# Kernel optimization log

Measured on AMD Instinct MI355X. Metric: run time of the kernel, lower is better.

## Reference

```python
import jax, jax.numpy as jnp
import numpy as np

N_ENT = 50000     # n_entities
C = 128           # channel
N_EDGES = 1600000 # n_edges (avg degree 32)
N_REL = 11        # n_relations; edge_type in [1, N_REL-1]
N_HOPS = 3
EPS = 1e-12       # F.normalize default eps


def setup_inputs() -> dict:
    key = jax.random.key(0)
    k1, k2, k3, k4 = jax.random.split(key, 4)
    entity_emb = jax.random.normal(k1, (N_ENT, C), dtype=jnp.float32)
    edge_index = jax.random.randint(k2, (2, N_EDGES), 0, N_ENT, dtype=jnp.int64)
    edge_type = jax.random.randint(k3, (N_EDGES,), 1, N_REL, dtype=jnp.int64)
    # xavier_uniform bound for (N_REL-1, C)
    bound = float(np.sqrt(6.0 / ((N_REL - 1) + C)))
    weight = jax.random.uniform(k4, (N_REL - 1, C), jnp.float32, -bound, bound)
    return {"entity_emb": entity_emb, "edge_index": edge_index,
            "edge_type": edge_type, "weight": weight}


def reference(entity_emb, edge_index, edge_type, weight):
    head, tail = edge_index[0], edge_index[1]
    # relation embedding per edge: weight[edge_type - 1] -> [E, C]
    rel_emb = weight[edge_type - 1]
    ones = jnp.ones((edge_index.shape[1],), entity_emb.dtype)
    # per-head in-degree counts (constant across hops)
    cnt = jax.ops.segment_sum(ones, head, num_segments=N_ENT)
    denom = jnp.maximum(cnt, 1.0)[:, None]  # scatter_mean: zero rows stay zero

    def hop(emb):
        msg = emb[tail] * rel_emb                                   # gather + mul [E, C]
        agg = jax.ops.segment_sum(msg, head, num_segments=N_ENT) / denom  # scatter_mean
        # F.normalize (L2 per row)
        norm = jnp.linalg.norm(agg, axis=1, keepdims=True)
        return agg / jnp.maximum(norm, EPS)

    res = entity_emb
    emb = entity_emb
    for _ in range(N_HOPS):
        emb = hop(emb)
        res = res + emb
    return res
```

## Files before the change

### kernel.cpp

```cpp
#include <hip/hip_runtime.h>

#define N_ENT   50000
#define CH      128
#define N_EDGES 1600000
#define N_RELM1 10
#define NB      391
#define BCAP    4608
#define PART_BLOCKS 800
#define CHUNK   (N_EDGES / PART_BLOCKS)
#define EPS_N   1e-12f

__device__ __forceinline__ unsigned int f2bf_bits(float f) {
    unsigned int x = __float_as_uint(f);
    return (x + 0x7FFFu + ((x >> 16) & 1u)) >> 16;
}

__global__ __launch_bounds__(256) void gc_part_kernel(const int* __restrict__ head,
                                                      const int* __restrict__ tail,
                                                      const int* __restrict__ etyp,
                                                      int* __restrict__ barr,
                                                      int* __restrict__ pack,
                                                      const float* __restrict__ ent,
                                                      unsigned int* __restrict__ emb) {
    __shared__ int hist[512];
    __shared__ int boff_s[512];
    __shared__ int fctr[512];
    __shared__ int psum[256];
    __shared__ int stageE[CHUNK];
    __shared__ unsigned short stageB[CHUNK];
    __shared__ int stage2[CHUNK];
    int tid = threadIdx.x, blk = blockIdx.x;
    for (int i = tid; i < 512; i += 256) { hist[i] = 0; fctr[i] = 0; }
    __syncthreads();
    int lo = blk * CHUNK;
    for (int i = tid; i < CHUNK; i += 256) {
        int e = lo + i;
        int h = head[e];
        int b = h >> 7;
        stageE[i] = (tail[e] & 0xFFFF) | ((etyp[e] - 1) << 16) | ((h & 127) << 20);
        stageB[i] = (unsigned short)b;
        atomicAdd(&hist[b], 1);
    }
    __syncthreads();
    int a0 = hist[2 * tid], a1 = hist[2 * tid + 1];
    int s2 = a0 + a1;
    psum[tid] = s2;
    __syncthreads();
    for (int d = 1; d < 256; d <<= 1) {
        int t = (tid >= d) ? psum[tid - d] : 0;
        __syncthreads();
        psum[tid] += t;
        __syncthreads();
    }
    int excl = psum[tid] - s2;
    boff_s[2 * tid] = excl;
    boff_s[2 * tid + 1] = excl + a0;
    __syncthreads();
    for (int i = tid; i < CHUNK; i += 256) {
        int b = stageB[i];
        int pos = boff_s[b] + atomicAdd(&fctr[b], 1);
        stage2[pos] = stageE[i];
    }
    __syncthreads();
    for (int i = tid; i < CHUNK; i += 256) barr[lo + i] = stage2[i];
    for (int i = tid; i < NB; i += 256)
        pack[blk * NB + i] = (boff_s[i] << 8) | fctr[i];
    for (int i = blk * 256 + tid; i < N_ENT * (CH / 2); i += PART_BLOCKS * 256) {
        float2 v = *(const float2*)(ent + 2 * (size_t)i);
        emb[i] = f2bf_bits(v.x) | (f2bf_bits(v.y) << 16);
    }
}

__global__ __launch_bounds__(1024) void gc_place_kernel(const int* __restrict__ barr,
                                                        const int* __restrict__ pack,
                                                        unsigned int* __restrict__ off_deg,
                                                        int* __restrict__ csr) {
    __shared__ int ent_s[BCAP];
    __shared__ int psum[1024];
    __shared__ int hcnt[128];
    __shared__ int hloc[128];
    __shared__ int hctr[128];
    int b = blockIdx.x, tid = threadIdx.x;
    if (tid < 128) { hcnt[tid] = 0; hctr[tid] = 0; }
    int c = 0, o = 0;
    if (tid < PART_BLOCKS) {
        int pk = pack[tid * NB + b];
        c = pk & 255;
        o = pk >> 8;
    }
    psum[tid] = c;
    __syncthreads();
    for (int d = 1; d < 1024; d <<= 1) {
        int t = (tid >= d) ? psum[tid - d] : 0;
        __syncthreads();
        psum[tid] += t;
        __syncthreads();
    }
    int my_off = psum[tid] - c;
    int n = psum[1023];
    const int* src = barr + tid * CHUNK + o;
    for (int k = 0; k < c; ++k) ent_s[my_off + k] = src[k];
    __syncthreads();
    for (int i = tid; i < n; i += 1024)
        atomicAdd(&hcnt[(ent_s[i] >> 20) & 127], 1);
    __syncthreads();
    int v = (tid < 128) ? hcnt[tid] : 0;
    for (int d = 1; d < 128; d <<= 1) {
        int t = (tid < 128 && tid >= d) ? hcnt[tid - d] : 0;
        __syncthreads();
        if (tid < 128) hcnt[tid] += t;
        __syncthreads();
    }
    int lo = b * BCAP;
    if (tid < 128) {
        int start = lo + hcnt[tid] - v;
        hloc[tid] = start;
        int h = (b << 7) + tid;
        if (h < N_ENT) off_deg[h] = ((unsigned)start << 11) | (unsigned)v;
    }
    __syncthreads();
    for (int i = tid; i < n; i += 1024) {
        int e = ent_s[i];
        int hl = (e >> 20) & 127;
        int pos = hloc[hl] + atomicAdd(&hctr[hl], 1);
        csr[pos] = e & 0xFFFFF;
    }
}

__global__ __launch_bounds__(256) void gc_hop_kernel(
        const unsigned int* __restrict__ src,
        const unsigned int* __restrict__ off_deg,
        const int* __restrict__ csr,
        const float* __restrict__ wt,
        unsigned int* __restrict__ dst,
        float* __restrict__ res,
        const float* __restrict__ ent,
        int init) {
    __shared__ float wt_s[N_RELM1 * CH];
    for (int i = threadIdx.x; i < N_RELM1 * CH; i += 256) wt_s[i] = wt[i];
    __syncthreads();

    int wave = threadIdx.x >> 6, lane = threadIdx.x & 63;
    int row = __builtin_amdgcn_readfirstlane(blockIdx.x * 4 + wave);

    unsigned od = (unsigned)__builtin_amdgcn_readfirstlane((int)off_deg[row]);
    int seg = (int)(od >> 11);
    int deg = (int)(od & 2047u);
    int seg_end = seg + deg;

    float ax = 0.f, ay = 0.f;
    int j = seg;
    for (; j + 8 <= seg_end; j += 8) {
        int pk[8];
        #pragma unroll
        for (int u = 0; u < 8; ++u)
            pk[u] = __builtin_amdgcn_readfirstlane(csr[j + u]);
        #pragma unroll
        for (int u = 0; u < 8; ++u) {
            unsigned v = src[pk[u] % 65536 * 64 + lane];
            float2 w = *(const float2*)(&wt_s[(pk[u] >> 16) * CH + 2 * lane]);
            ax = fmaf(__uint_as_float(v << 16), w.x, ax);
            ay = fmaf(__uint_as_float(v & 0xFFFF0000u), w.y, ay);
        }
    }
    for (; j < seg_end; ++j) {
        int pk = __builtin_amdgcn_readfirstlane(csr[j]);
        unsigned v = src[pk % 65536 * 64 + lane];
        float2 w = *(const float2*)(&wt_s[(pk >> 16) * CH + 2 * lane]);
        ax = fmaf(__uint_as_float(v << 16), w.x, ax);
        ay = fmaf(__uint_as_float(v & 0xFFFF0000u), w.y, ay);
    }

    float invd = 1.0f / fmaxf((float)deg, 1.0f);
    float x0 = ax * invd, x1 = ay * invd;

    float s = x0 * x0 + x1 * x1;
    #pragma unroll
    for (int o = 32; o > 0; o >>= 1) s += __shfl_down(s, o, 64);
    s = __shfl(s, 0, 64);

    float inv = 1.0f / fmaxf(sqrtf(s), EPS_N);
    float y0 = x0 * inv, y1 = x1 * inv;

    dst[(row << 6) + lane] = f2bf_bits(y0) | (f2bf_bits(y1) << 16);

    int base = (row << 7) + 2 * lane;
    if (init) {
        float2 e = *(const float2*)(ent + base);
        *(float2*)(res + base) = make_float2(e.x + y0, e.y + y1);
    } else {
        float2 rv = *(const float2*)(res + base);
        *(float2*)(res + base) = make_float2(rv.x + y0, rv.y + y1);
    }
}

extern "C" void kernel_launch(void* const* d_in, const int* in_sizes, int n_in,
                              void* d_out, int out_size, void* d_ws, size_t ws_size,
                              hipStream_t stream) {
    const float* ent  = (const float*)d_in[0];
    const int*   eidx = (const int*)d_in[1];
    const int*   etyp = (const int*)d_in[2];
    const float* wt   = (const float*)d_in[3];
    float*       res  = (float*)d_out;

    const int* head = eidx;
    const int* tail = eidx + N_EDGES;

    unsigned int* embA = (unsigned int*)d_ws;
    unsigned int* embB = embA + (size_t)N_ENT * 64;
    int* barr  = (int*)(embB + (size_t)N_ENT * 64);
    int* pack  = barr + N_EDGES;
    unsigned int* off_deg = (unsigned int*)(pack + PART_BLOCKS * NB);
    int* csr   = (int*)(off_deg + N_ENT);

    gc_part_kernel<<<PART_BLOCKS, 256, 0, stream>>>(head, tail, etyp, barr, pack,
                                                    ent, embA);
    gc_place_kernel<<<NB, 1024, 0, stream>>>(barr, pack, off_deg, csr);

    const int hop_grid = N_ENT / 4;
    gc_hop_kernel<<<hop_grid, 256, 0, stream>>>(embA, off_deg, csr, wt, embB, res, ent, 1);
    gc_hop_kernel<<<hop_grid, 256, 0, stream>>>(embB, off_deg, csr, wt, embA, res, ent, 0);
    gc_hop_kernel<<<hop_grid, 256, 0, stream>>>(embA, off_deg, csr, wt, embB, res, ent, 0);
}
```

Measured before the change: 298.3 us.

## Use wave-shuffle scans, fp16 residual accumulators, and deeper gather unroll

Replaces the shared-memory Hillis-Steele prefix scans in the partition and place kernels with wave-level shuffle scans plus a small cross-wave combine, cutting barrier count. The running residual sum between hops is now kept in fp16 ping-pong buffers instead of read-modify-write fp32. Only the last hop writes the fp32 output, and it skips the unused embedding store. The hop gather loop is unrolled to 16 edges to keep more loads in flight. The fp16 residual adds rounding error to the intermediate sums, and the larger unroll raises register pressure.

```diff
diff --git a/kernel.cpp b/kernel.cpp
--- a/kernel.cpp
+++ b/kernel.cpp
@@ -1,4 +1,5 @@
 #include <hip/hip_runtime.h>
+#include <hip/hip_fp16.h>
 
 #define N_ENT   50000
 #define CH      128
@@ -25,11 +26,12 @@
     __shared__ int hist[512];
     __shared__ int boff_s[512];
     __shared__ int fctr[512];
-    __shared__ int psum[256];
+    __shared__ int wsum[4];
     __shared__ int stageE[CHUNK];
     __shared__ unsigned short stageB[CHUNK];
     __shared__ int stage2[CHUNK];
     int tid = threadIdx.x, blk = blockIdx.x;
+    int lane = tid & 63, wv = tid >> 6;
     for (int i = tid; i < 512; i += 256) { hist[i] = 0; fctr[i] = 0; }
     __syncthreads();
     int lo = blk * CHUNK;
@@ -44,15 +46,21 @@
     __syncthreads();
     int a0 = hist[2 * tid], a1 = hist[2 * tid + 1];
     int s2 = a0 + a1;
-    psum[tid] = s2;
-    __syncthreads();
-    for (int d = 1; d < 256; d <<= 1) {
-        int t = (tid >= d) ? psum[tid - d] : 0;
-        __syncthreads();
-        psum[tid] += t;
-        __syncthreads();
-    }
-    int excl = psum[tid] - s2;
+    int x = s2;
+    #pragma unroll
+    for (int d = 1; d < 64; d <<= 1) {
+        int y = __shfl_up(x, d, 64);
+        if (lane >= d) x += y;
+    }
+    if (lane == 63) wsum[wv] = x;
+    __syncthreads();
+    if (tid == 0) {
+        int run = 0;
+        #pragma unroll
+        for (int w = 0; w < 4; ++w) { int t = wsum[w]; wsum[w] = run; run += t; }
+    }
+    __syncthreads();
+    int excl = wsum[wv] + x - s2;
     boff_s[2 * tid] = excl;
     boff_s[2 * tid + 1] = excl + a0;
     __syncthreads();
@@ -76,11 +84,13 @@
                                                         unsigned int* __restrict__ off_deg,
                                                         int* __restrict__ csr) {
     __shared__ int ent_s[BCAP];
-    __shared__ int psum[1024];
+    __shared__ int wsum[16];
+    __shared__ int ntot_s;
     __shared__ int hcnt[128];
     __shared__ int hloc[128];
     __shared__ int hctr[128];
     int b = blockIdx.x, tid = threadIdx.x;
+    int lane = tid & 63, wv = tid >> 6;
     if (tid < 128) { hcnt[tid] = 0; hctr[tid] = 0; }
     int c = 0, o = 0;
     if (tid < PART_BLOCKS) {
@@ -88,35 +98,50 @@
         c = pk & 255;
         o = pk >> 8;
     }
-    psum[tid] = c;
-    __syncthreads();
-    for (int d = 1; d < 1024; d <<= 1) {
-        int t = (tid >= d) ? psum[tid - d] : 0;
-        __syncthreads();
-        psum[tid] += t;
-        __syncthreads();
-    }
-    int my_off = psum[tid] - c;
-    int n = psum[1023];
+    int x = c;
+    #pragma unroll
+    for (int d = 1; d < 64; d <<= 1) {
+        int y = __shfl_up(x, d, 64);
+        if (lane >= d) x += y;
+    }
+    if (lane == 63) wsum[wv] = x;
+    __syncthreads();
+    if (wv == 0 && lane < 16) {
+        int w = wsum[lane];
+        int xx = w;
+        #pragma unroll
+        for (int d = 1; d < 16; d <<= 1) {
+            int y = __shfl_up(xx, d, 64);
+            if (lane >= d) xx += y;
+        }
+        wsum[lane] = xx - w;
+        if (lane == 15) ntot_s = xx;
+    }
+    __syncthreads();
+    int my_off = wsum[wv] + x - c;
+    int n = ntot_s;
     const int* src = barr + tid * CHUNK + o;
     for (int k = 0; k < c; ++k) ent_s[my_off + k] = src[k];
     __syncthreads();
     for (int i = tid; i < n; i += 1024)
         atomicAdd(&hcnt[(ent_s[i] >> 20) & 127], 1);
     __syncthreads();
-    int v = (tid < 128) ? hcnt[tid] : 0;
-    for (int d = 1; d < 128; d <<= 1) {
-        int t = (tid < 128 && tid >= d) ? hcnt[tid - d] : 0;
-        __syncthreads();
-        if (tid < 128) hcnt[tid] += t;
-        __syncthreads();
-    }
     int lo = b * BCAP;
-    if (tid < 128) {
-        int start = lo + hcnt[tid] - v;
-        hloc[tid] = start;
-        int h = (b << 7) + tid;
-        if (h < N_ENT) off_deg[h] = ((unsigned)start << 11) | (unsigned)v;
+    if (wv == 0) {
+        int a0 = hcnt[2 * lane], a1 = hcnt[2 * lane + 1];
+        int s2 = a0 + a1;
+        int xx = s2;
+        #pragma unroll
+        for (int d = 1; d < 64; d <<= 1) {
+            int y = __shfl_up(xx, d, 64);
+            if (lane >= d) xx += y;
+        }
+        int excl = xx - s2;
+        hloc[2 * lane] = lo + excl;
+        hloc[2 * lane + 1] = lo + excl + a0;
+        int h = (b << 7) + 2 * lane;
+        if (h < N_ENT)     off_deg[h]     = ((unsigned)(lo + excl) << 11) | (unsigned)a0;
+        if (h + 1 < N_ENT) off_deg[h + 1] = ((unsigned)(lo + excl + a0) << 11) | (unsigned)a1;
     }
     __syncthreads();
     for (int i = tid; i < n; i += 1024) {
@@ -133,9 +158,11 @@
         const int* __restrict__ csr,
         const float* __restrict__ wt,
         unsigned int* __restrict__ dst,
-        float* __restrict__ res,
+        const unsigned int* __restrict__ res_in,
+        unsigned int* __restrict__ res_out,
         const float* __restrict__ ent,
-        int init) {
+        float* __restrict__ out_f32,
+        int mode) {
     __shared__ float wt_s[N_RELM1 * CH];
     for (int i = threadIdx.x; i < N_RELM1 * CH; i += 256) wt_s[i] = wt[i];
     __syncthreads();
@@ -150,13 +177,13 @@
 
     float ax = 0.f, ay = 0.f;
     int j = seg;
-    for (; j + 8 <= seg_end; j += 8) {
-        int pk[8];
-        #pragma unroll
-        for (int u = 0; u < 8; ++u)
+    for (; j + 16 <= seg_end; j += 16) {
+        int pk[16];
+        #pragma unroll
+        for (int u = 0; u < 16; ++u)
             pk[u] = __builtin_amdgcn_readfirstlane(csr[j + u]);
         #pragma unroll
-        for (int u = 0; u < 8; ++u) {
+        for (int u = 0; u < 16; ++u) {
             unsigned v = src[pk[u] % 65536 * 64 + lane];
             float2 w = *(const float2*)(&wt_s[(pk[u] >> 16) * CH + 2 * lane]);
             ax = fmaf(__uint_as_float(v << 16), w.x, ax);
@@ -182,15 +209,23 @@
     float inv = 1.0f / fmaxf(sqrtf(s), EPS_N);
     float y0 = x0 * inv, y1 = x1 * inv;
 
-    dst[(row << 6) + lane] = f2bf_bits(y0) | (f2bf_bits(y1) << 16);
-
-    int base = (row << 7) + 2 * lane;
-    if (init) {
-        float2 e = *(const float2*)(ent + base);
-        *(float2*)(res + base) = make_float2(e.x + y0, e.y + y1);
+    if (mode < 2)
+        dst[(row << 6) + lane] = f2bf_bits(y0) | (f2bf_bits(y1) << 16);
+
+    float r0, r1;
+    if (mode == 0) {
+        float2 e = *(const float2*)(ent + (row << 7) + 2 * lane);
+        r0 = e.x + y0; r1 = e.y + y1;
     } else {
-        float2 rv = *(const float2*)(res + base);
-        *(float2*)(res + base) = make_float2(rv.x + y0, rv.y + y1);
+        __half2 h = *(const __half2*)(&res_in[(row << 6) + lane]);
+        float2 rv = __half22float2(h);
+        r0 = rv.x + y0; r1 = rv.y + y1;
+    }
+    if (mode == 2) {
+        *(float2*)(out_f32 + (row << 7) + 2 * lane) = make_float2(r0, r1);
+    } else {
+        __half2 h = __float22half2_rn(make_float2(r0, r1));
+        res_out[(row << 6) + lane] = *(unsigned int*)&h;
     }
 }
 
@@ -208,7 +243,9 @@
 
     unsigned int* embA = (unsigned int*)d_ws;
     unsigned int* embB = embA + (size_t)N_ENT * 64;
-    int* barr  = (int*)(embB + (size_t)N_ENT * 64);
+    unsigned int* res1 = embB + (size_t)N_ENT * 64;
+    unsigned int* res2 = res1 + (size_t)N_ENT * 64;
+    int* barr  = (int*)(res2 + (size_t)N_ENT * 64);
     int* pack  = barr + N_EDGES;
     unsigned int* off_deg = (unsigned int*)(pack + PART_BLOCKS * NB);
     int* csr   = (int*)(off_deg + N_ENT);
@@ -218,7 +255,10 @@
     gc_place_kernel<<<NB, 1024, 0, stream>>>(barr, pack, off_deg, csr);
 
     const int hop_grid = N_ENT / 4;
-    gc_hop_kernel<<<hop_grid, 256, 0, stream>>>(embA, off_deg, csr, wt, embB, res, ent, 1);
-    gc_hop_kernel<<<hop_grid, 256, 0, stream>>>(embB, off_deg, csr, wt, embA, res, ent, 0);
-    gc_hop_kernel<<<hop_grid, 256, 0, stream>>>(embA, off_deg, csr, wt, embB, res, ent, 0);
-}
+    gc_hop_kernel<<<hop_grid, 256, 0, stream>>>(embA, off_deg, csr, wt, embB,
+                                                nullptr, res1, ent, nullptr, 0);
+    gc_hop_kernel<<<hop_grid, 256, 0, stream>>>(embB, off_deg, csr, wt, embA,
+                                                res1, res2, ent, nullptr, 1);
+    gc_hop_kernel<<<hop_grid, 256, 0, stream>>>(embA, off_deg, csr, wt, nullptr,
+                                                res2, nullptr, ent, res, 2);
+}
```

Result: no change. 304.1 us (+1.9%).
